# Performance work log

Hardware: AMD Instinct MI355X
Metric: run time of the kernel (lower is better)

## Reference

```python
import jax, jax.numpy as jnp
import numpy as np

ALPHA, BETA, GAMMA, DELTA = 1.0, 1.0, 1.0, 0.001
DV, DD = 0.5, 1.5
N_INST = 8
EDGES_MAX = 512
EPS = 1e-12


def _safe_norm(sq):
    # sqrt of a sum-of-squares with a tiny eps for grad stability at 0
    return jnp.sqrt(jnp.maximum(sq, 0.0) + EPS)


def _per_image(feat, labels, label_edges):
    # feat: [P, C]; labels, label_edges: [P] int32 in [0, N_INST)
    P, C = feat.shape
    N = N_INST
    counts = jax.ops.segment_sum(jnp.ones((P,), feat.dtype), labels, num_segments=N)  # [N]
    means = jax.ops.segment_sum(feat, labels, num_segments=N) / counts[:, None]       # [N, C]

    # --- variance (pull) loss: per-pixel distance to its cluster mean ---
    d = _safe_norm(jnp.sum((feat - means[labels]) ** 2, axis=-1))  # [P]
    hinge = jax.nn.relu(d - DV) ** 2
    var_loss = jnp.sum(jax.ops.segment_sum(hinge, labels, num_segments=N) / counts) / N

    # --- distance (push) loss between cluster means, upper triangle ---
    diff = means[:, None, :] - means[None, :, :]
    dm = _safe_norm(jnp.sum(diff ** 2, axis=-1))  # [N, N]
    triu = jnp.triu(jnp.ones((N, N), dtype=bool), k=1)
    dist_loss = jnp.sum(jnp.where(triu, jax.nn.relu(2.0 * DD - dm) ** 2, 0.0)) / (N * (N - 1))

    # --- edge loss: first EDGES_MAX boundary pixels per instance (deterministic subsample) ---
    pix = jnp.arange(P, dtype=feat.dtype)
    def first_members(i):
        score = jnp.where(label_edges == i, -pix, -jnp.inf)
        _, idx = jax.lax.top_k(score, EDGES_MAX)
        return idx
    sel = jax.vmap(first_members)(jnp.arange(N))  # [N, E]
    eb = feat[sel.reshape(-1)]                    # [N*E, C]
    sq = jnp.sum(eb ** 2, axis=-1)
    d2 = sq[:, None] + sq[None, :] - 2.0 * (eb @ eb.T)  # [N*E, N*E] squared dists
    pd = _safe_norm(d2)
    pv = jax.nn.relu(2.0 * (DD - DV) - pd) ** 2
    pair = pv.reshape(N, EDGES_MAX, N, EDGES_MAX).sum(axis=(1, 3)) / (EDGES_MAX * EDGES_MAX)
    edge_loss = jnp.sum(jnp.where(triu, pair, 0.0)) / (N * (N - 1))

    # --- regularization on cluster means ---
    reg_loss = jnp.mean(_safe_norm(jnp.sum(means ** 2, axis=-1)))
    return var_loss, dist_loss, edge_loss, reg_loss


def setup_inputs() -> dict:
    key = jax.random.key(0)
    k1, k2, k3 = jax.random.split(key, 3)
    B, C, H, W = 4, 32, 512, 512
    features = jax.random.normal(k1, (B, C, H, W), jnp.float32)
    labels = jax.random.randint(k2, (B, H, W), 0, N_INST, jnp.int32)
    labelEdges = jax.random.randint(k3, (B, H, W), 0, N_INST, jnp.int32)
    return {"features": features, "labels": labels, "labelEdges": labelEdges}


def reference(features, labels, labelEdges):
    B, C, H, W = features.shape
    feat = features.transpose(0, 2, 3, 1).reshape(B, H * W, C)
    lab = labels.reshape(B, -1)
    le = labelEdges.reshape(B, -1)
    v, d, e, r = jax.vmap(_per_image)(feat, lab, le)
    varLoss = ALPHA * jnp.sum(v)
    distLoss = BETA * jnp.sum(d)
    edgeLoss = GAMMA * jnp.sum(e)
    regLoss = DELTA * jnp.sum(r)
    totalLoss = varLoss + distLoss + edgeLoss + regLoss
    return (totalLoss, varLoss, distLoss, edgeLoss, regLoss)
```

## Files before the change

kernel.cpp:

```cpp
#include <hip/hip_runtime.h>

#define NB 4
#define NC 32
#define NPIX 262144
#define NI 8
#define NE 512
#define FEPS 1e-12f

#define WS_SUMS   0
#define WS_CNT    1024
#define WS_HINGE  1056
#define WS_EDGE   1088
#define WS_ZERO_N 1089
#define WS_SEL    2048
#define WS_EB     20480
#define WS_SQ     544768

typedef __bf16 bf16x8 __attribute__((ext_vector_type(8)));
typedef float  f32x4  __attribute__((ext_vector_type(4)));

static __device__ __forceinline__ unsigned short f2bf(float x) {
    unsigned u = __builtin_bit_cast(unsigned, x);
    u += 0x7FFF + ((u >> 16) & 1);
    return (unsigned short)(u >> 16);
}

__global__ __launch_bounds__(256) void k_zero(float* __restrict__ ws) {
    int i = blockIdx.x * 256 + threadIdx.x;
    if (i < WS_ZERO_N) ws[i] = 0.f;
}

__global__ __launch_bounds__(256, 4) void k_seg_sums(const float* __restrict__ feat,
                                                     const int* __restrict__ lab,
                                                     float* __restrict__ sums,
                                                     float* __restrict__ cnts) {
    int tid = threadIdx.x;
    int lane = tid & 63, w = tid >> 6;
    int blk = blockIdx.x;
    int b = blk >> 9, rem = blk & 511;
    int cb = rem >> 1, h = rem & 1;
    int ch0 = h * 16 + w * 4;
    const float* fb = feat + ((size_t)b * NC + ch0) * NPIX + cb * 1024;
    const int*   lb = lab + (size_t)b * NPIX + cb * 1024;
    bool docnt = (w == 0) && (h == 0);

    float r[32];
#pragma unroll
    for (int k = 0; k < 32; k++) r[k] = 0.f;
    float cnt[8] = {0.f, 0.f, 0.f, 0.f, 0.f, 0.f, 0.f, 0.f};

#define ACC_ELEM(lx, v0, v1, v2, v3)                         \
    do {                                                     \
        _Pragma("unroll")                                    \
        for (int bin = 0; bin < 8; ++bin) {                  \
            float mk = ((lx) == bin) ? 1.f : 0.f;            \
            if (docnt) cnt[bin] += mk;                       \
            r[bin]      += mk * (v0);                        \
            r[8 + bin]  += mk * (v1);                        \
            r[16 + bin] += mk * (v2);                        \
            r[24 + bin] += mk * (v3);                        \
        }                                                    \
    } while (0)

    int4   lvA = *(const int4*)(lb + lane * 4);
    float4 fA0 = *(const float4*)(fb + 0 * (size_t)NPIX + lane * 4);
    float4 fA1 = *(const float4*)(fb + 1 * (size_t)NPIX + lane * 4);
    float4 fA2 = *(const float4*)(fb + 2 * (size_t)NPIX + lane * 4);
    float4 fA3 = *(const float4*)(fb + 3 * (size_t)NPIX + lane * 4);

#pragma unroll
    for (int g = 0; g < 4; g++) {
        int4 lvC = lvA;
        float4 c0 = fA0, c1 = fA1, c2 = fA2, c3 = fA3;
        if (g < 3) {
            int idx = (g + 1) * 256 + lane * 4;
            lvA = *(const int4*)(lb + idx);
            fA0 = *(const float4*)(fb + 0 * (size_t)NPIX + idx);
            fA1 = *(const float4*)(fb + 1 * (size_t)NPIX + idx);
            fA2 = *(const float4*)(fb + 2 * (size_t)NPIX + idx);
            fA3 = *(const float4*)(fb + 3 * (size_t)NPIX + idx);
        }
        ACC_ELEM(lvC.x, c0.x, c1.x, c2.x, c3.x);
        ACC_ELEM(lvC.y, c0.y, c1.y, c2.y, c3.y);
        ACC_ELEM(lvC.z, c0.z, c1.z, c2.z, c3.z);
        ACC_ELEM(lvC.w, c0.w, c1.w, c2.w, c3.w);
    }
#undef ACC_ELEM

#pragma unroll
    for (int k = 0; k < 32; k++) r[k] += __shfl_xor(r[k], 32);
#pragma unroll
    for (int half = 16; half >= 1; half >>= 1) {
#pragma unroll
        for (int k = 0; k < half; k++) {
            float t0 = __shfl_xor(r[k], half);
            float t1 = __shfl_xor(r[k + half], half);
            r[k] = (lane & half) ? (r[k + half] + t1) : (r[k] + t0);
        }
    }
    if (lane < 32)
        atomicAdd(&sums[((size_t)b * NI + (lane & 7)) * NC + ch0 + (lane >> 3)], r[0]);

    if (docnt) {
#pragma unroll
        for (int m = 8; m <= 32; m <<= 1) {
#pragma unroll
            for (int bin = 0; bin < 8; bin++) cnt[bin] += __shfl_xor(cnt[bin], m);
        }
#pragma unroll
        for (int half = 4; half >= 1; half >>= 1) {
#pragma unroll
            for (int k = 0; k < half; k++) {
                float t0 = __shfl_xor(cnt[k], half);
                float t1 = __shfl_xor(cnt[k + half], half);
                cnt[k] = (lane & half) ? (cnt[k + half] + t1) : (cnt[k] + t0);
            }
        }
        if (lane < 8) atomicAdd(&cnts[b * NI + lane], cnt[0]);
    }
}

__global__ __launch_bounds__(256, 4) void k_var(const float* __restrict__ feat,
                                                const int* __restrict__ lab,
                                                const float* __restrict__ sums,
                                                const float* __restrict__ cnts,
                                                float* __restrict__ hinge) {
    __shared__ float mlds[NI][33];
    __shared__ float hred[4][8];
    int tid = threadIdx.x;
    int lane = tid & 63, w = tid >> 6;
    int b = blockIdx.x >> 8, cb = blockIdx.x & 255;
    {
        int i = tid >> 5, c = tid & 31;
        mlds[i][c] = sums[(b * NI + i) * NC + c] / cnts[b * NI + i];
    }
    __syncthreads();

    int idx = tid * 4;
    int4 lv = *(const int4*)(lab + (size_t)b * NPIX + cb * 1024 + idx);
    const float* fb = feat + (size_t)b * NC * NPIX + cb * 1024 + idx;
    float ax = 0.f, ay = 0.f, az = 0.f, aw = 0.f;

    float4 FA[8], FB[8];
#define LOADF(BUF, CC)                                                          \
    do {                                                                        \
        _Pragma("unroll")                                                       \
        for (int u = 0; u < 8; ++u)                                             \
            BUF[u] = *(const float4*)(fb + (size_t)((CC) + u) * NPIX);          \
    } while (0)
#define CONSUME(BUF, CC)                                                        \
    do {                                                                        \
        _Pragma("unroll")                                                       \
        for (int u = 0; u < 8; ++u) {                                           \
            int c = (CC) + u;                                                   \
            float d;                                                            \
            d = BUF[u].x - mlds[lv.x][c]; ax += d * d;                          \
            d = BUF[u].y - mlds[lv.y][c]; ay += d * d;                          \
            d = BUF[u].z - mlds[lv.z][c]; az += d * d;                          \
            d = BUF[u].w - mlds[lv.w][c]; aw += d * d;                          \
        }                                                                       \
    } while (0)

    LOADF(FA, 0);
    LOADF(FB, 8);  CONSUME(FA, 0);
    LOADF(FA, 16); CONSUME(FB, 8);
    LOADF(FB, 24); CONSUME(FA, 16);
    CONSUME(FB, 24);
#undef LOADF
#undef CONSUME

    float t;
    t = fmaxf(sqrtf(ax + FEPS) - 0.5f, 0.f); float hx = t * t;
    t = fmaxf(sqrtf(ay + FEPS) - 0.5f, 0.f); float hy = t * t;
    t = fmaxf(sqrtf(az + FEPS) - 0.5f, 0.f); float hz = t * t;
    t = fmaxf(sqrtf(aw + FEPS) - 0.5f, 0.f); float hw = t * t;

    float hacc[8];
#pragma unroll
    for (int bin = 0; bin < 8; bin++)
        hacc[bin] = ((lv.x == bin) ? hx : 0.f) + ((lv.y == bin) ? hy : 0.f)
                  + ((lv.z == bin) ? hz : 0.f) + ((lv.w == bin) ? hw : 0.f);
#pragma unroll
    for (int m = 8; m <= 32; m <<= 1) {
#pragma unroll
        for (int bin = 0; bin < 8; bin++) hacc[bin] += __shfl_xor(hacc[bin], m);
    }
#pragma unroll
    for (int half = 4; half >= 1; half >>= 1) {
#pragma unroll
        for (int k = 0; k < half; k++) {
            float t0 = __shfl_xor(hacc[k], half);
            float t1 = __shfl_xor(hacc[k + half], half);
            hacc[k] = (lane & half) ? (hacc[k + half] + t1) : (hacc[k] + t0);
        }
    }
    if (lane < 8) hred[w][lane] = hacc[0];
    __syncthreads();
    if (tid < 8)
        atomicAdd(&hinge[b * NI + tid],
                  hred[0][tid] + hred[1][tid] + hred[2][tid] + hred[3][tid]);
}

__global__ __launch_bounds__(64) void k_sel(const int* __restrict__ le, int* __restrict__ sel) {
    int inst = blockIdx.x & 7;
    int b = blockIdx.x >> 3;
    int lane = threadIdx.x;
    const int* lp = le + (size_t)b * NPIX;
    int* sp = sel + blockIdx.x * NE;
    int s = 0;
    for (int base = 0; base < NPIX && s < NE; base += 256) {
        int4 l = *(const int4*)(lp + base + lane * 4);
        int m0 = (l.x == inst), m1 = (l.y == inst), m2 = (l.z == inst), m3 = (l.w == inst);
        int cnt = m0 + m1 + m2 + m3;
        int incl = cnt;
#pragma unroll
        for (int off = 1; off < 64; off <<= 1) {
            int t = __shfl_up(incl, off);
            if (lane >= off) incl += t;
        }
        int r = incl - cnt;
        int pbase = base + lane * 4;
        if (m0) { if (s + r < NE) sp[s + r] = pbase + 0; r++; }
        if (m1) { if (s + r < NE) sp[s + r] = pbase + 1; r++; }
        if (m2) { if (s + r < NE) sp[s + r] = pbase + 2; r++; }
        if (m3) { if (s + r < NE) sp[s + r] = pbase + 3; r++; }
        s += __shfl(incl, 63);
    }
    for (int idx = s + lane; idx < NE; idx += 64) sp[idx] = 0;
}

__global__ __launch_bounds__(256) void k_gather(const float* __restrict__ feat,
                                                const int* __restrict__ sel,
                                                short* __restrict__ ebh,
                                                float* __restrict__ sq) {
    int oct = blockIdx.x;
    int bi = blockIdx.y;
    int b = bi >> 3;
    int tid = threadIdx.x;
    int rrel = tid >> 2, qc = tid & 3;
    int r = bi * NE + oct * 64 + rrel;
    int p = sel[r];
    const float* fp = feat + (size_t)b * NC * NPIX + p;
    int c0 = qc * 8;
    float s = 0.f;
    int pk[4];
#pragma unroll
    for (int j = 0; j < 4; j++) {
        float v0 = fp[(size_t)(c0 + 2 * j) * NPIX];
        float v1 = fp[(size_t)(c0 + 2 * j + 1) * NPIX];
        s += v0 * v0 + v1 * v1;
        pk[j] = (unsigned)f2bf(v0) | ((unsigned)f2bf(v1) << 16);
    }
    *(int4*)(ebh + (size_t)r * NC + c0) = make_int4(pk[0], pk[1], pk[2], pk[3]);
    s += __shfl_xor(s, 1);
    s += __shfl_xor(s, 2);
    if (qc == 0) sq[r] = s;
}

__global__ __launch_bounds__(256) void k_edge(const short* __restrict__ ebh,
                                              const float* __restrict__ sq,
                                              float* __restrict__ edge_acc) {
    __shared__ float sqa[128], sqb[128];
    __shared__ float wsum[4];
    int tid = threadIdx.x;
    int lane = tid & 63, w = tid >> 6;
    int ti = blockIdx.x >> 2, tj = blockIdx.x & 3;
    int q = blockIdx.y;
    int b = blockIdx.z;
    int pi = 0, pj = 0, k = q;
    for (int i = 0; i < 8; i++) { int row = 7 - i; if (k < row) { pi = i; pj = i + 1 + k; break; } k -= row; }
    int base_a = b * 4096 + pi * NE + ti * 128;
    int base_b = b * 4096 + pj * NE + tj * 128;

    if (tid < 128) sqa[tid] = sq[base_a + tid];
    else sqb[tid - 128] = sq[base_b + tid - 128];
    __syncthreads();

    int lrow = lane & 15;
    int lk = (lane >> 4) * 8;

    bf16x8 a[2];
#pragma unroll
    for (int u = 0; u < 2; u++)
        a[u] = *(const bf16x8*)(ebh + (size_t)(base_a + w * 32 + u * 16 + lrow) * NC + lk);
    bf16x8 bb[8];
#pragma unroll
    for (int v = 0; v < 8; v++)
        bb[v] = *(const bf16x8*)(ebh + (size_t)(base_b + v * 16 + lrow) * NC + lk);

    f32x4 acc[2][8];
#pragma unroll
    for (int u = 0; u < 2; u++)
#pragma unroll
        for (int v = 0; v < 8; v++) acc[u][v] = (f32x4){0.f, 0.f, 0.f, 0.f};

#pragma unroll
    for (int u = 0; u < 2; u++)
#pragma unroll
        for (int v = 0; v < 8; v++)
            acc[u][v] = __builtin_amdgcn_mfma_f32_16x16x32_bf16(a[u], bb[v], acc[u][v], 0, 0, 0);

    float lsum = 0.f;
    int orow0 = w * 32 + (lane >> 4) * 4;
    int ocol = lane & 15;
#pragma unroll
    for (int u = 0; u < 2; u++) {
#pragma unroll
        for (int v = 0; v < 8; v++) {
            float sb = sqb[v * 16 + ocol];
#pragma unroll
            for (int rg = 0; rg < 4; rg++) {
                float d2 = sqa[orow0 + u * 16 + rg] + sb - 2.f * acc[u][v][rg];
                float pd = sqrtf(fmaxf(d2, 0.f) + FEPS);
                float t = 2.f - pd;
                if (t > 0.f) lsum += t * t;
            }
        }
    }
#pragma unroll
    for (int off = 32; off > 0; off >>= 1) lsum += __shfl_xor(lsum, off);
    if (lane == 0) wsum[w] = lsum;
    __syncthreads();
    if (tid == 0) atomicAdd(edge_acc, wsum[0] + wsum[1] + wsum[2] + wsum[3]);
}

__global__ __launch_bounds__(256) void k_final(const float* __restrict__ sums,
                                               const float* __restrict__ cnts,
                                               const float* __restrict__ hinge,
                                               const float* __restrict__ edge_acc,
                                               float* __restrict__ out) {
    __shared__ float m[NB * NI * NC];
    __shared__ float accs[3];
    int tid = threadIdx.x;
    if (tid < 3) accs[tid] = 0.f;
    for (int i = tid; i < NB * NI * NC; i += 256) m[i] = sums[i] / cnts[i >> 5];
    __syncthreads();

    float var_p = 0.f, dist_p = 0.f, reg_p = 0.f;
    if (tid < 32) {
        var_p = hinge[tid] / cnts[tid] * (1.f / 8.f);
        const float* mm = &m[tid * NC];
        float s = 0.f;
        for (int c = 0; c < NC; c++) s += mm[c] * mm[c];
        reg_p = sqrtf(s + FEPS) * (0.001f / 8.f);
    }
    if (tid < NB * 28) {
        int b = tid / 28, q = tid % 28;
        int pi = 0, pj = 0, k = q;
        for (int i = 0; i < 8; i++) { int row = 7 - i; if (k < row) { pi = i; pj = i + 1 + k; break; } k -= row; }
        const float* ma = &m[(b * NI + pi) * NC];
        const float* mb = &m[(b * NI + pj) * NC];
        float s = 0.f;
        for (int c = 0; c < NC; c++) { float d = ma[c] - mb[c]; s += d * d; }
        float dm = sqrtf(s + FEPS);
        float t = fmaxf(3.0f - dm, 0.f);
        dist_p = t * t * (1.f / 56.f);
    }
    atomicAdd(&accs[0], var_p);
    atomicAdd(&accs[1], dist_p);
    atomicAdd(&accs[2], reg_p);
    __syncthreads();
    if (tid == 0) {
        float var = accs[0], dist = accs[1], reg = accs[2];
        float edge = edge_acc[0] * (1.f / (512.f * 512.f * 56.f));
        out[0] = var + dist + edge + reg;
        out[1] = var;
        out[2] = dist;
        out[3] = edge;
        out[4] = reg;
    }
}

extern "C" void kernel_launch(void* const* d_in, const int* in_sizes, int n_in,
                              void* d_out, int out_size, void* d_ws, size_t ws_size,
                              hipStream_t stream) {
    const float* feat   = (const float*)d_in[0];
    const int*   labels = (const int*)d_in[1];
    const int*   le     = (const int*)d_in[2];
    float* out = (float*)d_out;
    float* ws  = (float*)d_ws;

    float* sums  = ws + WS_SUMS;
    float* cnts  = ws + WS_CNT;
    float* hinge = ws + WS_HINGE;
    float* edge  = ws + WS_EDGE;
    int*   sel   = (int*)(ws + WS_SEL);
    short* ebh   = (short*)(ws + WS_EB);
    float* sq    = ws + WS_SQ;

    hipLaunchKernelGGL(k_zero,     dim3(5),           dim3(256), 0, stream, ws);
    hipLaunchKernelGGL(k_seg_sums, dim3(2048),        dim3(256), 0, stream, feat, labels, sums, cnts);
    hipLaunchKernelGGL(k_var,      dim3(1024),        dim3(256), 0, stream, feat, labels, sums, cnts, hinge);
    hipLaunchKernelGGL(k_sel,      dim3(32),          dim3(64),  0, stream, le, sel);
    hipLaunchKernelGGL(k_gather,   dim3(8, 32),       dim3(256), 0, stream, feat, sel, ebh, sq);
    hipLaunchKernelGGL(k_edge,     dim3(16, 28, 4),   dim3(256), 0, stream, ebh, sq, edge);
    hipLaunchKernelGGL(k_final,    dim3(1),           dim3(256), 0, stream, sums, cnts, hinge, edge, out);
}
```

Before: 318.3 us.

## Compute segment sums with bf16 MFMA one-hot matmul and sharded atomics

Rewrites the segmented feature sum as a one-hot-mask times features matrix multiply on MFMA, with features cast to bf16. Partial sums go to 8 shard copies to cut atomic contention, and those shards are reduced in k_var and k_final. k_var is retiled to 2 pixels per thread over twice as many blocks. The bf16 rounding of features lowers the precision of the cluster means.

```diff
diff --git a/kernel.cpp b/kernel.cpp
--- a/kernel.cpp
+++ b/kernel.cpp
@@ -6,15 +6,17 @@
 #define NI 8
 #define NE 512
 #define FEPS 1e-12f
+#define NSH 8
 
 #define WS_SUMS   0
-#define WS_CNT    1024
 #define WS_HINGE  1056
 #define WS_EDGE   1088
-#define WS_ZERO_N 1089
-#define WS_SEL    2048
-#define WS_EB     20480
-#define WS_SQ     544768
+#define WS_PSUM   1152
+#define WS_PCNT   9344
+#define WS_ZERO_N 9600
+#define WS_SEL    10240
+#define WS_EB     28672
+#define WS_SQ     294912
 
 typedef __bf16 bf16x8 __attribute__((ext_vector_type(8)));
 typedef float  f32x4  __attribute__((ext_vector_type(4)));
@@ -32,154 +34,112 @@
 
 __global__ __launch_bounds__(256, 4) void k_seg_sums(const float* __restrict__ feat,
                                                      const int* __restrict__ lab,
-                                                     float* __restrict__ sums,
-                                                     float* __restrict__ cnts) {
-    int tid = threadIdx.x;
-    int lane = tid & 63, w = tid >> 6;
+                                                     float* __restrict__ psums,
+                                                     float* __restrict__ pcnts) {
+    __shared__ float sred[4][NI][33];
+    __shared__ float cred[4][NI];
+    int tid = threadIdx.x, lane = tid & 63, w = tid >> 6;
     int blk = blockIdx.x;
-    int b = blk >> 9, rem = blk & 511;
-    int cb = rem >> 1, h = rem & 1;
-    int ch0 = h * 16 + w * 4;
-    const float* fb = feat + ((size_t)b * NC + ch0) * NPIX + cb * 1024;
-    const int*   lb = lab + (size_t)b * NPIX + cb * 1024;
-    bool docnt = (w == 0) && (h == 0);
-
-    float r[32];
-#pragma unroll
-    for (int k = 0; k < 32; k++) r[k] = 0.f;
-    float cnt[8] = {0.f, 0.f, 0.f, 0.f, 0.f, 0.f, 0.f, 0.f};
-
-#define ACC_ELEM(lx, v0, v1, v2, v3)                         \
-    do {                                                     \
-        _Pragma("unroll")                                    \
-        for (int bin = 0; bin < 8; ++bin) {                  \
-            float mk = ((lx) == bin) ? 1.f : 0.f;            \
-            if (docnt) cnt[bin] += mk;                       \
-            r[bin]      += mk * (v0);                        \
-            r[8 + bin]  += mk * (v1);                        \
-            r[16 + bin] += mk * (v2);                        \
-            r[24 + bin] += mk * (v3);                        \
-        }                                                    \
-    } while (0)
-
-    int4   lvA = *(const int4*)(lb + lane * 4);
-    float4 fA0 = *(const float4*)(fb + 0 * (size_t)NPIX + lane * 4);
-    float4 fA1 = *(const float4*)(fb + 1 * (size_t)NPIX + lane * 4);
-    float4 fA2 = *(const float4*)(fb + 2 * (size_t)NPIX + lane * 4);
-    float4 fA3 = *(const float4*)(fb + 3 * (size_t)NPIX + lane * 4);
-
-#pragma unroll
-    for (int g = 0; g < 4; g++) {
-        int4 lvC = lvA;
-        float4 c0 = fA0, c1 = fA1, c2 = fA2, c3 = fA3;
-        if (g < 3) {
-            int idx = (g + 1) * 256 + lane * 4;
-            lvA = *(const int4*)(lb + idx);
-            fA0 = *(const float4*)(fb + 0 * (size_t)NPIX + idx);
-            fA1 = *(const float4*)(fb + 1 * (size_t)NPIX + idx);
-            fA2 = *(const float4*)(fb + 2 * (size_t)NPIX + idx);
-            fA3 = *(const float4*)(fb + 3 * (size_t)NPIX + idx);
-        }
-        ACC_ELEM(lvC.x, c0.x, c1.x, c2.x, c3.x);
-        ACC_ELEM(lvC.y, c0.y, c1.y, c2.y, c3.y);
-        ACC_ELEM(lvC.z, c0.z, c1.z, c2.z, c3.z);
-        ACC_ELEM(lvC.w, c0.w, c1.w, c2.w, c3.w);
-    }
-#undef ACC_ELEM
-
-#pragma unroll
-    for (int k = 0; k < 32; k++) r[k] += __shfl_xor(r[k], 32);
-#pragma unroll
-    for (int half = 16; half >= 1; half >>= 1) {
-#pragma unroll
-        for (int k = 0; k < half; k++) {
-            float t0 = __shfl_xor(r[k], half);
-            float t1 = __shfl_xor(r[k + half], half);
-            r[k] = (lane & half) ? (r[k + half] + t1) : (r[k] + t0);
-        }
-    }
-    if (lane < 32)
-        atomicAdd(&sums[((size_t)b * NI + (lane & 7)) * NC + ch0 + (lane >> 3)], r[0]);
-
-    if (docnt) {
-#pragma unroll
-        for (int m = 8; m <= 32; m <<= 1) {
-#pragma unroll
-            for (int bin = 0; bin < 8; bin++) cnt[bin] += __shfl_xor(cnt[bin], m);
-        }
-#pragma unroll
-        for (int half = 4; half >= 1; half >>= 1) {
-#pragma unroll
-            for (int k = 0; k < half; k++) {
-                float t0 = __shfl_xor(cnt[k], half);
-                float t1 = __shfl_xor(cnt[k + half], half);
-                cnt[k] = (lane & half) ? (cnt[k + half] + t1) : (cnt[k] + t0);
-            }
-        }
-        if (lane < 8) atomicAdd(&cnts[b * NI + lane], cnt[0]);
-    }
+    int b = blk >> 9, chunk = blk & 511;
+    int p0 = chunk * 512 + w * 128;
+    int kg = lane >> 4, rc = lane & 15;
+    const int* lb = lab + (size_t)b * NPIX;
+    const float* f0 = feat + ((size_t)b * NC + rc) * NPIX;
+    const float* f1 = feat + ((size_t)b * NC + 16 + rc) * NPIX;
+
+    f32x4 acc0 = {0.f, 0.f, 0.f, 0.f}, acc1 = {0.f, 0.f, 0.f, 0.f};
+    float cnt = 0.f;
+
+#pragma unroll 2
+    for (int it = 0; it < 4; it++) {
+        int p = p0 + it * 32 + kg * 8;
+        int4 la = *(const int4*)(lb + p);
+        int4 lc = *(const int4*)(lb + p + 4);
+        float4 a0 = *(const float4*)(f0 + p);
+        float4 a1 = *(const float4*)(f0 + p + 4);
+        float4 b0 = *(const float4*)(f1 + p);
+        float4 b1 = *(const float4*)(f1 + p + 4);
+
+        uint4 mu;
+        mu.x = (la.x == rc ? 0x3F80u : 0u) | (la.y == rc ? 0x3F800000u : 0u);
+        mu.y = (la.z == rc ? 0x3F80u : 0u) | (la.w == rc ? 0x3F800000u : 0u);
+        mu.z = (lc.x == rc ? 0x3F80u : 0u) | (lc.y == rc ? 0x3F800000u : 0u);
+        mu.w = (lc.z == rc ? 0x3F80u : 0u) | (lc.w == rc ? 0x3F800000u : 0u);
+        cnt += (float)((la.x == rc) + (la.y == rc) + (la.z == rc) + (la.w == rc)
+                     + (lc.x == rc) + (lc.y == rc) + (lc.z == rc) + (lc.w == rc));
+        bf16x8 af = __builtin_bit_cast(bf16x8, mu);
+        bf16x8 bf0 = {(__bf16)a0.x, (__bf16)a0.y, (__bf16)a0.z, (__bf16)a0.w,
+                      (__bf16)a1.x, (__bf16)a1.y, (__bf16)a1.z, (__bf16)a1.w};
+        bf16x8 bf1 = {(__bf16)b0.x, (__bf16)b0.y, (__bf16)b0.z, (__bf16)b0.w,
+                      (__bf16)b1.x, (__bf16)b1.y, (__bf16)b1.z, (__bf16)b1.w};
+        acc0 = __builtin_amdgcn_mfma_f32_16x16x32_bf16(af, bf0, acc0, 0, 0, 0);
+        acc1 = __builtin_amdgcn_mfma_f32_16x16x32_bf16(af, bf1, acc1, 0, 0, 0);
+    }
+
+    if (lane < 32) {
+#pragma unroll
+        for (int rg = 0; rg < 4; rg++) {
+            int row = (lane >> 4) * 4 + rg;
+            sred[w][row][rc] = acc0[rg];
+            sred[w][row][16 + rc] = acc1[rg];
+        }
+    }
+    cnt += __shfl_xor(cnt, 16);
+    cnt += __shfl_xor(cnt, 32);
+    if (lane < 8) cred[w][lane] = cnt;
+    __syncthreads();
+
+    int sh = blk & (NSH - 1);
+    {
+        int bin = tid >> 5, ch = tid & 31;
+        float s = sred[0][bin][ch] + sred[1][bin][ch] + sred[2][bin][ch] + sred[3][bin][ch];
+        atomicAdd(&psums[sh * (NB * NI * NC) + ((size_t)b * NI + bin) * NC + ch], s);
+    }
+    if (tid < 8)
+        atomicAdd(&pcnts[sh * (NB * NI) + b * NI + tid],
+                  cred[0][tid] + cred[1][tid] + cred[2][tid] + cred[3][tid]);
 }
 
 __global__ __launch_bounds__(256, 4) void k_var(const float* __restrict__ feat,
                                                 const int* __restrict__ lab,
-                                                const float* __restrict__ sums,
-                                                const float* __restrict__ cnts,
+                                                const float* __restrict__ psums,
+                                                const float* __restrict__ pcnts,
                                                 float* __restrict__ hinge) {
     __shared__ float mlds[NI][33];
     __shared__ float hred[4][8];
-    int tid = threadIdx.x;
-    int lane = tid & 63, w = tid >> 6;
-    int b = blockIdx.x >> 8, cb = blockIdx.x & 255;
+    int tid = threadIdx.x, lane = tid & 63, w = tid >> 6;
+    int blk = blockIdx.x;
+    int b = blk >> 9, chunk = blk & 511;
     {
-        int i = tid >> 5, c = tid & 31;
-        mlds[i][c] = sums[(b * NI + i) * NC + c] / cnts[b * NI + i];
-    }
-    __syncthreads();
-
-    int idx = tid * 4;
-    int4 lv = *(const int4*)(lab + (size_t)b * NPIX + cb * 1024 + idx);
-    const float* fb = feat + (size_t)b * NC * NPIX + cb * 1024 + idx;
-    float ax = 0.f, ay = 0.f, az = 0.f, aw = 0.f;
-
-    float4 FA[8], FB[8];
-#define LOADF(BUF, CC)                                                          \
-    do {                                                                        \
-        _Pragma("unroll")                                                       \
-        for (int u = 0; u < 8; ++u)                                             \
-            BUF[u] = *(const float4*)(fb + (size_t)((CC) + u) * NPIX);          \
-    } while (0)
-#define CONSUME(BUF, CC)                                                        \
-    do {                                                                        \
-        _Pragma("unroll")                                                       \
-        for (int u = 0; u < 8; ++u) {                                           \
-            int c = (CC) + u;                                                   \
-            float d;                                                            \
-            d = BUF[u].x - mlds[lv.x][c]; ax += d * d;                          \
-            d = BUF[u].y - mlds[lv.y][c]; ay += d * d;                          \
-            d = BUF[u].z - mlds[lv.z][c]; az += d * d;                          \
-            d = BUF[u].w - mlds[lv.w][c]; aw += d * d;                          \
-        }                                                                       \
-    } while (0)
-
-    LOADF(FA, 0);
-    LOADF(FB, 8);  CONSUME(FA, 0);
-    LOADF(FA, 16); CONSUME(FB, 8);
-    LOADF(FB, 24); CONSUME(FA, 16);
-    CONSUME(FB, 24);
-#undef LOADF
-#undef CONSUME
-
+        int bin = tid >> 5, ch = tid & 31;
+        float s = 0.f, c = 0.f;
+#pragma unroll
+        for (int sh = 0; sh < NSH; sh++) {
+            s += psums[sh * (NB * NI * NC) + ((size_t)b * NI + bin) * NC + ch];
+            c += pcnts[sh * (NB * NI) + b * NI + bin];
+        }
+        mlds[bin][ch] = s / c;
+    }
+    __syncthreads();
+
+    int p0 = chunk * 512 + tid * 2;
+    int2 lv = *(const int2*)(lab + (size_t)b * NPIX + p0);
+    const float* fb = feat + (size_t)b * NC * NPIX + p0;
+    float a0 = 0.f, a1 = 0.f;
+#pragma unroll
+    for (int c = 0; c < NC; c++) {
+        float2 f = *(const float2*)(fb + (size_t)c * NPIX);
+        float d0 = f.x - mlds[lv.x][c]; a0 += d0 * d0;
+        float d1 = f.y - mlds[lv.y][c]; a1 += d1 * d1;
+    }
     float t;
-    t = fmaxf(sqrtf(ax + FEPS) - 0.5f, 0.f); float hx = t * t;
-    t = fmaxf(sqrtf(ay + FEPS) - 0.5f, 0.f); float hy = t * t;
-    t = fmaxf(sqrtf(az + FEPS) - 0.5f, 0.f); float hz = t * t;
-    t = fmaxf(sqrtf(aw + FEPS) - 0.5f, 0.f); float hw = t * t;
+    t = fmaxf(sqrtf(a0 + FEPS) - 0.5f, 0.f); float h0 = t * t;
+    t = fmaxf(sqrtf(a1 + FEPS) - 0.5f, 0.f); float h1 = t * t;
 
     float hacc[8];
 #pragma unroll
     for (int bin = 0; bin < 8; bin++)
-        hacc[bin] = ((lv.x == bin) ? hx : 0.f) + ((lv.y == bin) ? hy : 0.f)
-                  + ((lv.z == bin) ? hz : 0.f) + ((lv.w == bin) ? hw : 0.f);
+        hacc[bin] = ((lv.x == bin) ? h0 : 0.f) + ((lv.y == bin) ? h1 : 0.f);
 #pragma unroll
     for (int m = 8; m <= 32; m <<= 1) {
 #pragma unroll
@@ -324,21 +284,34 @@
     if (tid == 0) atomicAdd(edge_acc, wsum[0] + wsum[1] + wsum[2] + wsum[3]);
 }
 
-__global__ __launch_bounds__(256) void k_final(const float* __restrict__ sums,
-                                               const float* __restrict__ cnts,
+__global__ __launch_bounds__(256) void k_final(const float* __restrict__ psums,
+                                               const float* __restrict__ pcnts,
                                                const float* __restrict__ hinge,
                                                const float* __restrict__ edge_acc,
                                                float* __restrict__ out) {
     __shared__ float m[NB * NI * NC];
+    __shared__ float cshr[NB * NI];
     __shared__ float accs[3];
     int tid = threadIdx.x;
     if (tid < 3) accs[tid] = 0.f;
-    for (int i = tid; i < NB * NI * NC; i += 256) m[i] = sums[i] / cnts[i >> 5];
+    if (tid < NB * NI) {
+        float c = 0.f;
+#pragma unroll
+        for (int sh = 0; sh < NSH; sh++) c += pcnts[sh * (NB * NI) + tid];
+        cshr[tid] = c;
+    }
+    __syncthreads();
+    for (int i = tid; i < NB * NI * NC; i += 256) {
+        float s = 0.f;
+#pragma unroll
+        for (int sh = 0; sh < NSH; sh++) s += psums[sh * (NB * NI * NC) + i];
+        m[i] = s / cshr[i >> 5];
+    }
     __syncthreads();
 
     float var_p = 0.f, dist_p = 0.f, reg_p = 0.f;
     if (tid < 32) {
-        var_p = hinge[tid] / cnts[tid] * (1.f / 8.f);
+        var_p = hinge[tid] / cshr[tid] * (1.f / 8.f);
         const float* mm = &m[tid * NC];
         float s = 0.f;
         for (int c = 0; c < NC; c++) s += mm[c] * mm[c];
@@ -380,19 +353,19 @@
     float* out = (float*)d_out;
     float* ws  = (float*)d_ws;
 
-    float* sums  = ws + WS_SUMS;
-    float* cnts  = ws + WS_CNT;
     float* hinge = ws + WS_HINGE;
     float* edge  = ws + WS_EDGE;
+    float* psums = ws + WS_PSUM;
+    float* pcnts = ws + WS_PCNT;
     int*   sel   = (int*)(ws + WS_SEL);
     short* ebh   = (short*)(ws + WS_EB);
     float* sq    = ws + WS_SQ;
 
-    hipLaunchKernelGGL(k_zero,     dim3(5),           dim3(256), 0, stream, ws);
-    hipLaunchKernelGGL(k_seg_sums, dim3(2048),        dim3(256), 0, stream, feat, labels, sums, cnts);
-    hipLaunchKernelGGL(k_var,      dim3(1024),        dim3(256), 0, stream, feat, labels, sums, cnts, hinge);
+    hipLaunchKernelGGL(k_zero,     dim3(38),          dim3(256), 0, stream, ws);
+    hipLaunchKernelGGL(k_seg_sums, dim3(2048),        dim3(256), 0, stream, feat, labels, psums, pcnts);
+    hipLaunchKernelGGL(k_var,      dim3(2048),        dim3(256), 0, stream, feat, labels, psums, pcnts, hinge);
     hipLaunchKernelGGL(k_sel,      dim3(32),          dim3(64),  0, stream, le, sel);
     hipLaunchKernelGGL(k_gather,   dim3(8, 32),       dim3(256), 0, stream, feat, sel, ebh, sq);
     hipLaunchKernelGGL(k_edge,     dim3(16, 28, 4),   dim3(256), 0, stream, ebh, sq, edge);
-    hipLaunchKernelGGL(k_final,    dim3(1),           dim3(256), 0, stream, sums, cnts, hinge, edge, out);
-}
+    hipLaunchKernelGGL(k_final,    dim3(1),           dim3(256), 0, stream, psums, pcnts, hinge, edge, out);
+}
```

Result: faster. 286.9 us (-9.9%).
